# Optimization experiments

Hardware: AMD Instinct MI355X
Metric: run time of the kernel (lower is better)

## Reference

```python
import jax, jax.numpy as jnp
import numpy as np

N_NODES = 50000
N_EDGES = 600000
D_IN = 128
D_OUT = 128
P_DROP = 0.1
BN_EPS = 1e-5


def setup_inputs() -> dict:
    key = jax.random.key(0)
    ks = jax.random.split(key, 6)
    x = jax.random.normal(ks[0], (N_NODES, D_IN), dtype=jnp.float32)
    weight = jax.random.normal(ks[1], (D_IN, D_OUT), dtype=jnp.float32) * (1.0 / np.sqrt(D_IN))
    bias = jnp.zeros((D_OUT,), dtype=jnp.float32)
    gamma = jnp.ones((D_OUT,), dtype=jnp.float32)
    beta = jnp.zeros((D_OUT,), dtype=jnp.float32)
    dropout_u = jax.random.uniform(ks[2], (N_NODES, D_OUT), dtype=jnp.float32)
    edge_index = jax.random.randint(ks[3], (2, N_EDGES), 0, N_NODES, dtype=jnp.int64)
    return {"x": x, "weight": weight, "bias": bias, "gamma": gamma,
            "beta": beta, "dropout_u": dropout_u, "edge_index": edge_index}


def reference(x, weight, bias, gamma, beta, dropout_u, edge_index):
    N = x.shape[0]
    # --- GCNConv (add_self_loops=True, symmetric normalization) ---
    loop = jnp.arange(N, dtype=edge_index.dtype)
    src = jnp.concatenate([edge_index[0], loop])  # [E+N]
    dst = jnp.concatenate([edge_index[1], loop])  # [E+N]
    xw = x @ weight                               # [N, D_OUT] small GEMM
    deg = jnp.zeros((N,), dtype=xw.dtype).at[dst].add(1.0)
    dinv = jnp.where(deg > 0, jax.lax.rsqrt(jnp.maximum(deg, 1.0)), 0.0)
    norm = dinv[src] * dinv[dst]                  # [E+N]
    msgs = xw[src] * norm[:, None]                # gather: [E+N, D_OUT]
    z = jax.ops.segment_sum(msgs, dst, num_segments=N) + bias
    # --- activation -> BatchNorm (training stats) -> dropout ---
    z = jax.nn.relu(z)
    mean = jnp.mean(z, axis=0)
    var = jnp.mean((z - mean) ** 2, axis=0)       # biased var, as BN uses
    z = (z - mean) * jax.lax.rsqrt(var + BN_EPS) * gamma + beta
    keep = (dropout_u > P_DROP).astype(z.dtype)
    z = z * keep * (1.0 / (1.0 - P_DROP))
    return z.astype(x.dtype)
```

## Files before the change

kernel.cpp:

```cpp
#include <hip/hip_runtime.h>
#include <cstdint>
#include <cstddef>

#define D 128
#define P_DROP 0.1f
#define INV_KEEP (1.0f / 0.9f)
#define BN_EPS 1e-5f

typedef __attribute__((ext_vector_type(8))) short bf16x8;
typedef __attribute__((ext_vector_type(4))) float f32x4;

__device__ __forceinline__ unsigned f2bf(float f) {
    unsigned u = __float_as_uint(f);
    return (u + 0x7fffu + ((u >> 16) & 1u)) >> 16;
}
__device__ __forceinline__ float bf_lo(unsigned v) { return __uint_as_float(v << 16); }
__device__ __forceinline__ float bf_hi(unsigned v) { return __uint_as_float(v & 0xffff0000u); }

__global__ void k_init(int* __restrict__ hist, int N,
                       float* __restrict__ bnacc,
                       int* __restrict__ ssrc, int PS,
                       unsigned short* __restrict__ xwb) {
    int stride = gridDim.x * blockDim.x;
    int i0 = blockIdx.x * blockDim.x + threadIdx.x;
    for (int i = i0; i < PS; i += stride) ssrc[i] = N;
    for (int i = i0; i < N; i += stride) hist[i] = 0;
    if (i0 < 256) bnacc[i0] = 0.f;
    if (i0 < 64) ((unsigned*)(xwb + (size_t)N * D))[i0] = 0u;
}

__global__ void k_hist(const int* __restrict__ dst, int* __restrict__ hist, int E) {
    int i = blockIdx.x * blockDim.x + threadIdx.x;
    if (i < E) atomicAdd(&hist[dst[i]], 1);
}

__global__ void k_scanA(const int* __restrict__ hist, int* __restrict__ tmp,
                        int* __restrict__ blocksum, int N) {
    __shared__ int sd[256];
    int tid = threadIdx.x;
    int i = blockIdx.x * 256 + tid;
    sd[tid] = (i < N) ? ((hist[i] + 7) & ~7) : 0;
    __syncthreads();
    for (int o = 1; o < 256; o <<= 1) {
        int t = (tid >= o) ? sd[tid - o] : 0;
        __syncthreads();
        sd[tid] += t;
        __syncthreads();
    }
    tmp[i] = sd[tid];
    if (tid == 255) blocksum[blockIdx.x] = sd[255];
}

__global__ void k_scanBC(const int* __restrict__ tmp, const int* __restrict__ blocksum,
                         const int* __restrict__ hist,
                         int* __restrict__ rowptr, int* __restrict__ cursor,
                         int N, int NBLK) {
    __shared__ int sd[256];
    int tid = threadIdx.x;
    int b = blockIdx.x;
    sd[tid] = (tid < NBLK && tid < b) ? blocksum[tid] : 0;
    __syncthreads();
    for (int o = 128; o > 0; o >>= 1) {
        if (tid < o) sd[tid] += sd[tid + o];
        __syncthreads();
    }
    int boff = sd[0];
    int i = b * 256 + tid;
    if (i < N) {
        int pd = (hist[i] + 7) & ~7;
        int r = tmp[i] + boff - pd;
        rowptr[i] = r;
        cursor[i] = r;
    }
}

__global__ void k_place(const int* __restrict__ src, const int* __restrict__ dst,
                        int* __restrict__ cursor, int* __restrict__ ssrc, int E) {
    int i = blockIdx.x * blockDim.x + threadIdx.x;
    if (i < E) {
        int d = dst[i];
        int p = atomicAdd(&cursor[d], 1);
        ssrc[p] = src[i];
    }
}

__global__ __launch_bounds__(256) void k_gemm(
    const float* __restrict__ x, const float* __restrict__ w,
    const int* __restrict__ hist, unsigned short* __restrict__ xwb,
    float* __restrict__ dinv, int N) {
    __shared__ unsigned short xs[64][136];
    __shared__ unsigned short wt[128][136];
    int tid = threadIdx.x;
    int row0 = blockIdx.x * 64;

#pragma unroll
    for (int i = 0; i < 32; ++i) {
        int flat = tid + i * 256;
        int n = flat & 127;
        int kp = flat >> 7;
        float a0 = w[(size_t)(2 * kp) * D + n];
        float a1 = w[(size_t)(2 * kp + 1) * D + n];
        *(unsigned*)&wt[n][2 * kp] = f2bf(a0) | (f2bf(a1) << 16);
    }
#pragma unroll
    for (int i = 0; i < 8; ++i) {
        int flat = tid + i * 256;
        int r = flat >> 5;
        int kq = flat & 31;
        int row = row0 + r;
        float4 v = (row < N) ? *(const float4*)&x[(size_t)row * D + kq * 4]
                             : make_float4(0.f, 0.f, 0.f, 0.f);
        uint2 pk;
        pk.x = f2bf(v.x) | (f2bf(v.y) << 16);
        pk.y = f2bf(v.z) | (f2bf(v.w) << 16);
        *(uint2*)&xs[r][kq * 4] = pk;
    }
    __syncthreads();

    int wv = tid >> 6, lane = tid & 63;
    int l15 = lane & 15, quad = lane >> 4;
    int mrow = wv * 16 + l15;
    f32x4 acc[8];
#pragma unroll
    for (int t = 0; t < 8; ++t) acc[t] = (f32x4){0.f, 0.f, 0.f, 0.f};
#pragma unroll
    for (int k0 = 0; k0 < D; k0 += 32) {
        bf16x8 af = *(bf16x8*)&xs[mrow][k0 + quad * 8];
#pragma unroll
        for (int nt = 0; nt < 8; ++nt) {
            bf16x8 bfr = *(bf16x8*)&wt[nt * 16 + l15][k0 + quad * 8];
            acc[nt] = __builtin_amdgcn_mfma_f32_16x16x32_bf16(af, bfr, acc[nt], 0, 0, 0);
        }
    }
#pragma unroll
    for (int reg = 0; reg < 4; ++reg) {
        int node = row0 + wv * 16 + quad * 4 + reg;
        if (node < N) {
            float dv = rsqrtf((float)(hist[node] + 1));
            if (l15 == 0) dinv[node] = dv;
#pragma unroll
            for (int nt = 0; nt < 8; ++nt) {
                float val = acc[nt][reg] * dv;
                xwb[(size_t)node * D + nt * 16 + l15] = (unsigned short)f2bf(val);
            }
        }
    }
}

__global__ __launch_bounds__(256) void k_aggregate(
    const unsigned short* __restrict__ xwb, const float* __restrict__ dinv,
    const int* __restrict__ ssrc, const int* __restrict__ rowptr,
    const int* __restrict__ hist, const float* __restrict__ bias,
    float* __restrict__ y, float* __restrict__ bnacc, int N) {
    int tid = threadIdx.x;
    int lane = tid & 63;
    int wv = tid >> 6;
    int w0 = blockIdx.x * 4 + wv;
    int totw = gridDim.x * 4;
    float2 b2 = *(const float2*)(bias + lane * 2);
    float s0 = 0.f, s1 = 0.f, q0 = 0.f, q1 = 0.f;

    for (int n = w0; n < N; n += totw) {
        int nn = __builtin_amdgcn_readfirstlane(n);
        int base = rowptr[nn];
        int deg = hist[nn];
        int pdeg = (deg + 7) & ~7;
        unsigned sv = *(const unsigned*)(xwb + (size_t)nn * D + lane * 2);
        float a0 = bf_lo(sv), a1 = bf_hi(sv);

        for (int c0 = 0; c0 < pdeg; c0 += 64) {
            int vsrc = ssrc[base + c0 + lane];
            int lim = min(64, pdeg - c0);
            for (int j0 = 0; j0 < lim; j0 += 8) {
                unsigned vr[8];
#pragma unroll
                for (int j = 0; j < 8; ++j) {
                    int idx = __builtin_amdgcn_readlane(vsrc, j0 + j);
                    vr[j] = *(const unsigned*)(xwb + (size_t)idx * D + lane * 2);
                }
#pragma unroll
                for (int j = 0; j < 8; ++j) { a0 += bf_lo(vr[j]); a1 += bf_hi(vr[j]); }
            }
        }
        float dv = dinv[nn];
        float z0 = fmaxf(fmaf(a0, dv, b2.x), 0.f);
        float z1 = fmaxf(fmaf(a1, dv, b2.y), 0.f);
        *(float2*)(y + (size_t)nn * D + lane * 2) = make_float2(z0, z1);
        s0 += z0; s1 += z1; q0 += z0 * z0; q1 += z1 * z1;
    }

    __shared__ float red[256][4];
    red[tid][0] = s0; red[tid][1] = s1; red[tid][2] = q0; red[tid][3] = q1;
    __syncthreads();
    int o = tid;
    int col = o & 127;
    int l = col >> 1;
    int si = ((o >= 128) ? 2 : 0) + (col & 1);
    float acc = red[0 * 64 + l][si] + red[1 * 64 + l][si] +
                red[2 * 64 + l][si] + red[3 * 64 + l][si];
    atomicAdd(&bnacc[o], acc);
}

__global__ __launch_bounds__(256) void k_finalize(
    float* __restrict__ out, const float* __restrict__ u,
    const float* __restrict__ bnacc, const float* __restrict__ gamma,
    const float* __restrict__ beta, int total4, float invN) {
    __shared__ float sc[128], sh[128];
    int tid = threadIdx.x;
    if (tid < 128) {
        float mean = bnacc[tid] * invN;
        float var = fmaxf(bnacc[128 + tid] * invN - mean * mean, 0.f);
        float s = gamma[tid] * rsqrtf(var + BN_EPS);
        sc[tid] = s;
        sh[tid] = beta[tid] - mean * s;
    }
    __syncthreads();
    int stride = gridDim.x * 256;
    for (int i = blockIdx.x * 256 + tid; i < total4; i += stride) {
        float4 v = ((const float4*)out)[i];
        float4 uu = ((const float4*)u)[i];
        int c = (i & 31) * 4;
        v.x = fmaf(v.x, sc[c],     sh[c])     * (uu.x > P_DROP ? INV_KEEP : 0.f);
        v.y = fmaf(v.y, sc[c + 1], sh[c + 1]) * (uu.y > P_DROP ? INV_KEEP : 0.f);
        v.z = fmaf(v.z, sc[c + 2], sh[c + 2]) * (uu.z > P_DROP ? INV_KEEP : 0.f);
        v.w = fmaf(v.w, sc[c + 3], sh[c + 3]) * (uu.w > P_DROP ? INV_KEEP : 0.f);
        ((float4*)out)[i] = v;
    }
}

extern "C" void kernel_launch(void* const* d_in, const int* in_sizes, int n_in,
                              void* d_out, int out_size, void* d_ws, size_t ws_size,
                              hipStream_t stream) {
    const float* x      = (const float*)d_in[0];
    const float* weight = (const float*)d_in[1];
    const float* bias   = (const float*)d_in[2];
    const float* gamma  = (const float*)d_in[3];
    const float* beta   = (const float*)d_in[4];
    const float* du     = (const float*)d_in[5];
    const int*   eidx   = (const int*)d_in[6];
    float* out = (float*)d_out;

    const int N = in_sizes[0] / D;
    const int E = in_sizes[6] / 2;
    const int* esrc = eidx;
    const int* edst = eidx + E;

    char* p = (char*)d_ws;
    auto alloc = [&](size_t bytes) {
        char* q = p;
        p += (bytes + 255) & ~(size_t)255;
        return q;
    };
    unsigned short* xwb = (unsigned short*)alloc((size_t)(N + 1) * D * sizeof(unsigned short));
    int*   hist     = (int*)alloc((size_t)N * sizeof(int));
    int*   cursor   = (int*)alloc((size_t)N * sizeof(int));
    int*   rowptr   = (int*)alloc((size_t)N * sizeof(int));
    const int NBLK = (N + 255) / 256;
    int*   tmp      = (int*)alloc((size_t)NBLK * 256 * sizeof(int));
    int*   blocksum = (int*)alloc((size_t)NBLK * sizeof(int));
    const int PS = E + 7 * N + 64;
    int*   ssrc     = (int*)alloc((size_t)PS * sizeof(int));
    float* dinv     = (float*)alloc((size_t)N * sizeof(float));
    float* bnacc    = (float*)alloc(256 * sizeof(float));

    const int EB = (E + 255) / 256;
    const int total4 = N * (D / 4);

    hipLaunchKernelGGL(k_init, dim3(1024), dim3(256), 0, stream,
                       hist, N, bnacc, ssrc, PS, xwb);
    hipLaunchKernelGGL(k_hist, dim3(EB), dim3(256), 0, stream, edst, hist, E);
    hipLaunchKernelGGL(k_scanA, dim3(NBLK), dim3(256), 0, stream, hist, tmp, blocksum, N);
    hipLaunchKernelGGL(k_scanBC, dim3(NBLK), dim3(256), 0, stream,
                       tmp, blocksum, hist, rowptr, cursor, N, NBLK);
    hipLaunchKernelGGL(k_place, dim3(EB), dim3(256), 0, stream, esrc, edst, cursor, ssrc, E);
    hipLaunchKernelGGL(k_gemm, dim3((N + 63) / 64), dim3(256), 0, stream,
                       x, weight, hist, xwb, dinv, N);
    hipLaunchKernelGGL(k_aggregate, dim3(1024), dim3(256), 0, stream,
                       xwb, dinv, ssrc, rowptr, hist, bias, out, bnacc, N);
    hipLaunchKernelGGL(k_finalize, dim3(2048), dim3(256), 0, stream,
                       out, du, bnacc, gamma, beta, total4, 1.0f / (float)N);
}
```

Baseline: 238.0 us.

## Prefetch next node's CSR metadata and widen gather batch in aggregate

The aggregate kernel now software-pipelines each wave's node loop: rowptr, degree and the first 64 source indices of the next node are loaded while the current node is being gathered. The inner gather is unrolled to 16 outstanding row loads, with an 8-wide tail, to raise memory-level parallelism. The self-row load moves after the neighbour loop, and the grid doubles to 2048 blocks. The aim is to hide the dependent index-load latency between nodes, at the cost of more registers and possibly lower occupancy.

```diff
diff --git a/kernel.cpp b/kernel.cpp
--- a/kernel.cpp
+++ b/kernel.cpp
@@ -160,18 +160,41 @@
     float2 b2 = *(const float2*)(bias + lane * 2);
     float s0 = 0.f, s1 = 0.f, q0 = 0.f, q1 = 0.f;
 
-    for (int n = w0; n < N; n += totw) {
+    int n = w0;
+    int baseC = 0, degC = 0, vsC = 0;
+    if (n < N) {
+        baseC = rowptr[n];
+        degC = hist[n];
+        vsC = ssrc[baseC + lane];
+    }
+
+    while (n < N) {
         int nn = __builtin_amdgcn_readfirstlane(n);
-        int base = rowptr[nn];
-        int deg = hist[nn];
-        int pdeg = (deg + 7) & ~7;
-        unsigned sv = *(const unsigned*)(xwb + (size_t)nn * D + lane * 2);
-        float a0 = bf_lo(sv), a1 = bf_hi(sv);
-
+        int np = n + totw;
+        int baseP = 0, degP = 0, vsP = 0;
+        if (np < N) {
+            int npp = __builtin_amdgcn_readfirstlane(np);
+            baseP = rowptr[npp];
+            degP = hist[npp];
+            vsP = ssrc[baseP + lane];
+        }
+        int pdeg = (degC + 7) & ~7;
+        float a0 = 0.f, a1 = 0.f;
         for (int c0 = 0; c0 < pdeg; c0 += 64) {
-            int vsrc = ssrc[base + c0 + lane];
+            int vsrc = (c0 == 0) ? vsC : ssrc[baseC + c0 + lane];
             int lim = min(64, pdeg - c0);
-            for (int j0 = 0; j0 < lim; j0 += 8) {
+            int j0 = 0;
+            for (; j0 + 16 <= lim; j0 += 16) {
+                unsigned vr[16];
+#pragma unroll
+                for (int j = 0; j < 16; ++j) {
+                    int idx = __builtin_amdgcn_readlane(vsrc, j0 + j);
+                    vr[j] = *(const unsigned*)(xwb + (size_t)idx * D + lane * 2);
+                }
+#pragma unroll
+                for (int j = 0; j < 16; ++j) { a0 += bf_lo(vr[j]); a1 += bf_hi(vr[j]); }
+            }
+            if (j0 < lim) {
                 unsigned vr[8];
 #pragma unroll
                 for (int j = 0; j < 8; ++j) {
@@ -182,11 +205,14 @@
                 for (int j = 0; j < 8; ++j) { a0 += bf_lo(vr[j]); a1 += bf_hi(vr[j]); }
             }
         }
+        unsigned sv = *(const unsigned*)(xwb + (size_t)nn * D + lane * 2);
+        a0 += bf_lo(sv); a1 += bf_hi(sv);
         float dv = dinv[nn];
         float z0 = fmaxf(fmaf(a0, dv, b2.x), 0.f);
         float z1 = fmaxf(fmaf(a1, dv, b2.y), 0.f);
         *(float2*)(y + (size_t)nn * D + lane * 2) = make_float2(z0, z1);
         s0 += z0; s1 += z1; q0 += z0 * z0; q1 += z1 * z1;
+        n = np; baseC = baseP; degC = degP; vsC = vsP;
     }
 
     __shared__ float red[256][4];
@@ -275,7 +301,7 @@
     hipLaunchKernelGGL(k_place, dim3(EB), dim3(256), 0, stream, esrc, edst, cursor, ssrc, E);
     hipLaunchKernelGGL(k_gemm, dim3((N + 63) / 64), dim3(256), 0, stream,
                        x, weight, hist, xwb, dinv, N);
-    hipLaunchKernelGGL(k_aggregate, dim3(1024), dim3(256), 0, stream,
+    hipLaunchKernelGGL(k_aggregate, dim3(2048), dim3(256), 0, stream,
                        xwb, dinv, ssrc, rowptr, hist, bias, out, bnacc, N);
     hipLaunchKernelGGL(k_finalize, dim3(2048), dim3(256), 0, stream,
                        out, du, bnacc, gamma, beta, total4, 1.0f / (float)N);
```

New measurement: 260.1 us. 1.09x slower.
